# Kernel optimization log

Measured on AMD Instinct MI355X. Metric: run time of the kernel, lower is better.

The kernel has to match this reference:

```python
import jax, jax.numpy as jnp
import numpy as np

NUM_HEADS = 12
ROPE_THETA = 100.0

def _rotate_half(x):
    x1 = x[..., ::2]
    x2 = x[..., 1::2]
    return jnp.stack((-x2, x1), axis=-1).reshape(x.shape)

def _apply_rope(x, cos, sin):
    return x * cos + _rotate_half(x) * sin

def _rope_cos_sin(h, w, head_dim, theta):
    quarter = head_dim // 4  # head_dim=64 -> 16 freq bands
    inv_freq = 1.0 / theta ** (jnp.arange(quarter, dtype=jnp.float32) / max(quarter, 1))
    y = jnp.repeat(jnp.arange(h, dtype=jnp.float32), w)   # [h*w]
    xc = jnp.tile(jnp.arange(w, dtype=jnp.float32), h)    # [h*w]
    y_freqs = y[:, None] * inv_freq[None, :]               # [N, quarter]
    x_freqs = xc[:, None] * inv_freq[None, :]
    y_ang = jnp.repeat(y_freqs, 2, axis=-1)                # [N, half]
    x_ang = jnp.repeat(x_freqs, 2, axis=-1)
    ang = jnp.concatenate([y_ang, x_ang], axis=-1)         # [N, head_dim]
    return jnp.cos(ang)[None, None], jnp.sin(ang)[None, None]  # [1,1,N,hd]

def setup_inputs() -> dict:
    key = jax.random.key(0)
    ks = jax.random.split(key, 8)
    B, S, D = 8, 1025, 768
    s = 0.02
    return {
        "x": jax.random.normal(ks[0], (B, S, D), jnp.float32),
        "q_w": jax.random.normal(ks[1], (D, D), jnp.float32) * s,
        "q_b": jax.random.normal(ks[2], (D,), jnp.float32) * s,
        "k_w": jax.random.normal(ks[3], (D, D), jnp.float32) * s,
        "v_w": jax.random.normal(ks[4], (D, D), jnp.float32) * s,
        "v_b": jax.random.normal(ks[5], (D,), jnp.float32) * s,
        "o_w": jax.random.normal(ks[6], (D, D), jnp.float32) * s,
        "o_b": jax.random.normal(ks[7], (D,), jnp.float32) * s,
        "h": 32,
        "w": 32,
        "num_prefix_tokens": 1,
    }

def reference(x, q_w, q_b, k_w, v_w, v_b, o_w, o_b, h, w, num_prefix_tokens):
    B, S, D = x.shape
    H = NUM_HEADS
    hd = D // H
    scale = hd ** -0.5
    p = num_prefix_tokens

    def proj(W, b):
        y = jnp.einsum('bsd,ed->bse', x, W)
        if b is not None:
            y = y + b
        return y.reshape(B, S, H, hd).transpose(0, 2, 1, 3)  # [B,H,S,hd]

    q = proj(q_w, q_b)
    k = proj(k_w, None)
    v = proj(v_w, v_b)

    cos, sin = _rope_cos_sin(h, w, hd, ROPE_THETA)
    q = jnp.concatenate([q[:, :, :p], _apply_rope(q[:, :, p:], cos, sin)], axis=2)
    k = jnp.concatenate([k[:, :, :p], _apply_rope(k[:, :, p:], cos, sin)], axis=2)

    attn = jnp.einsum('bhqd,bhkd->bhqk', q * scale, k)
    attn = jax.nn.softmax(attn, axis=-1)
    out = jnp.einsum('bhqk,bhkd->bhqd', attn, v)
    out = out.transpose(0, 2, 1, 3).reshape(B, S, D)
    return jnp.einsum('bsd,ed->bse', out, o_w) + o_b
```

## Files before the change

### kernel.cpp

```cpp
#include <hip/hip_runtime.h>

typedef unsigned short u16;
typedef unsigned int   u32;
typedef __attribute__((ext_vector_type(4))) short s4;
typedef __attribute__((ext_vector_type(8))) short s8;
typedef __attribute__((ext_vector_type(4))) float f4;
typedef __attribute__((ext_vector_type(16))) float f16v;

#define NB   8
#define SEQ  1025
#define DIM  768
#define NH   12
#define HD   64
#define BPAD 1040
#define MPAD 8320
#define MV   8200
#define SQP  1040
#define SKP  1088
#define NG16 68
#define NQKV 2304
#define BHT  96
#define QSCALE 0.1803368801111204f

__device__ __forceinline__ u16 f2bf(float f) {
  u32 u = __builtin_bit_cast(u32, f);
  u += 0x7fffu + ((u >> 16) & 1u);
  return (u16)(u >> 16);
}
__device__ __forceinline__ float bf2f(u16 h) {
  return __builtin_bit_cast(float, ((u32)h) << 16);
}
__device__ __forceinline__ float exp2f_(float x) {
#if __has_builtin(__builtin_amdgcn_exp2f)
  return __builtin_amdgcn_exp2f(x);
#else
  return exp2f(x);
#endif
}
__device__ __forceinline__ u32 cvtpk(float a, float b) {
  u32 r;
  asm("v_cvt_pk_bf16_f32 %0, %1, %2" : "=v"(r) : "v"(a), "v"(b));
  return r;
}

typedef const __attribute__((address_space(1))) void cas1v;
typedef __attribute__((address_space(3))) void as3v;
__device__ __forceinline__ void gload16(const void* g, void* l) {
  __builtin_amdgcn_global_load_lds((cas1v*)g, (as3v*)l, 16, 0, 0);
}

#define MFMA16(a, b, c) __builtin_amdgcn_mfma_f32_16x16x32_bf16(a, b, c, 0, 0, 0)
#define MFMA32(a, b, c) __builtin_amdgcn_mfma_f32_32x32x16_bf16(a, b, c, 0, 0, 0)

__global__ void conv_all(const float* __restrict__ x,
                         const float* __restrict__ qw, const float* __restrict__ kw,
                         const float* __restrict__ vw, const float* __restrict__ ow,
                         const float* __restrict__ qb, const float* __restrict__ vb,
                         u16* __restrict__ xb,
                         u16* __restrict__ wqkv, u16* __restrict__ wo,
                         float* __restrict__ biasq, float2* __restrict__ rt) {
  if (blockIdx.x < 6240) {
    int i = blockIdx.x * 256 + threadIdx.x;
    int e = i * 4;
    int row = e / DIM, col = e - row * DIM;
    int b = row / BPAD, s = row - b * BPAD;
    s4 o;
    if (s < SEQ) {
      float4 v = *(const float4*)(x + ((size_t)(b * SEQ + s)) * DIM + col);
      o[0] = (short)f2bf(v.x); o[1] = (short)f2bf(v.y);
      o[2] = (short)f2bf(v.z); o[3] = (short)f2bf(v.w);
    } else {
      o = (s4){0, 0, 0, 0};
    }
    *(s4*)(xb + e) = o;
  } else {
    int i = (blockIdx.x - 6240) * 256 + threadIdx.x;
    wqkv[i]           = f2bf(qw[i]);
    wqkv[i + 589824]  = f2bf(kw[i]);
    wqkv[i + 1179648] = f2bf(vw[i]);
    wo[i]             = f2bf(ow[i]);
    if (i < NQKV) biasq[i] = (i < 768) ? qb[i] : (i < 1536 ? 0.f : vb[i - 1536]);
    if (i < SEQ * 32) {
      int s = i >> 5, jj = i & 31;
      float cs = 1.f, sn = 0.f;
      if (s > 0) {
        int tok = s - 1;
        int pos = (jj < 16) ? (tok >> 5) : (tok & 31);
        int f = jj & 15;
        float ang = (float)pos * __expf((float)f * -0.28782313662425572f);
        __sincosf(ang, &sn, &cs);
      }
      rt[i] = make_float2(cs, sn);
    }
  }
}

__global__ __launch_bounds__(512, 4) void gemm_qkv(const u16* __restrict__ A, const u16* __restrict__ Bm,
                                                   const float* __restrict__ bias,
                                                   u16* __restrict__ Ql, u16* __restrict__ Kl,
                                                   u16* __restrict__ Vp, const float2* __restrict__ rt) {
  __shared__ u16 smem[24576];
  const int K = DIM;
  int tid = threadIdx.x;
  int lane = tid & 63, wave = tid >> 6;
  int g = lane >> 4, c16 = lane & 15;
  int wm = wave >> 2, wn = wave & 3;
  int nwg = gridDim.x, orig = blockIdx.x;
  int qd = nwg >> 3, rm = nwg & 7, xcd = orig & 7;
  int wgid = (xcd < rm ? xcd * (qd + 1) : rm * (qd + 1) + (xcd - rm) * qd) + (orig >> 3);
  int m0 = (wgid / 9) * 128, n0 = (wgid % 9) * 256;
  f4 acc[4][4] = {};

  int ldrow = wave * 16 + (lane >> 2);
  int ldk = ((lane & 3) ^ ((ldrow >> 1) & 3)) * 8;
  const u16* Asrc = A + (size_t)(m0 + ldrow) * K + ldk;
  const u16* Bsrc = Bm + (size_t)(n0 + ldrow) * K + ldk;

  auto stage = [&](int buf, int k0) {
    gload16(Asrc + k0,           smem + buf * 4096 + wave * 512);
    gload16(Bsrc + k0,           smem + 8192 + buf * 8192 + wave * 512);
    gload16(Bsrc + 128 * K + k0, smem + 8192 + buf * 8192 + 4096 + wave * 512);
  };

  stage(0, 0);
  __syncthreads();
  int kx = (g ^ ((c16 >> 1) & 3)) * 8;
  for (int t = 0; t < 24; t++) {
    int buf = t & 1;
    if (t + 1 < 24) stage(buf ^ 1, (t + 1) << 5);
    s8 af[4], bf[4];
#pragma unroll
    for (int i = 0; i < 4; i++) {
      af[i] = *(const s8*)(smem + buf * 4096 + (wm * 64 + i * 16 + c16) * 32 + kx);
      bf[i] = *(const s8*)(smem + 8192 + buf * 8192 + (wn * 64 + i * 16 + c16) * 32 + kx);
    }
    __builtin_amdgcn_s_setprio(1);
#pragma unroll
    for (int i = 0; i < 4; i++)
#pragma unroll
      for (int j = 0; j < 4; j++)
        acc[i][j] = MFMA16(af[i], bf[j], acc[i][j]);
    __builtin_amdgcn_s_setprio(0);
    __syncthreads();
  }

  int part = (n0 >= 1536) ? 2 : (n0 >= 768 ? 1 : 0);
  float qs = (part == 0) ? QSCALE : 1.0f;
  u16 (*ct)[258] = (u16(*)[258])smem;
#pragma unroll
  for (int ih = 0; ih < 2; ih++) {
    __syncthreads();
#pragma unroll
    for (int j = 0; j < 4; j++) {
      int col = wn * 64 + j * 16 + c16;
      float bv = bias[n0 + col];
      int jj = (col & 63) >> 1;
      int odd = col & 1;
#pragma unroll
      for (int il = 0; il < 2; il++) {
        int i = ih * 2 + il;
        int lrow = wm * 32 + il * 16 + g * 4;
        int mrow = m0 + wm * 64 + i * 16 + g * 4;
#pragma unroll
        for (int r = 0; r < 4; r++) {
          float v = acc[i][j][r] + bv;
          u16 o;
          if (part < 2) {
            float vp = __shfl_xor(v, 1);
            int s = (mrow + r) % BPAD;
            float2 t = rt[(s < SEQ ? s : SEQ - 1) * 32 + jj];
            float rv = odd ? (v * t.x + vp * t.y) : (v * t.x - vp * t.y);
            o = f2bf(rv * qs);
          } else {
            o = f2bf(v);
          }
          ct[lrow + r][col] = o;
        }
      }
    }
    __syncthreads();
    if (part < 2) {
      u16* dstB = (part == 0) ? Ql : Kl;
      int stride = (part == 0) ? SQP : SKP;
#pragma unroll
      for (int p = 0; p < 4; p++) {
        int task = p * 512 + tid;
        int lrow = task >> 5, cg = (task & 31) * 8;
        int m = m0 + (lrow >> 5) * 64 + ih * 32 + (lrow & 31);
        int b = m / BPAD, s = m - b * BPAD;
        int n = n0 + cg;
        int hq = (n >> 6) - part * NH;
        s8 v = *(const s8*)&ct[lrow][cg];
        *(s8*)(dstB + ((size_t)((b * NH + hq) * stride + s)) * HD + (n & 63)) = v;
      }
    } else {
#pragma unroll
      for (int p = 0; p < 2; p++) {
        int task = p * 512 + tid;
        int col = task & 255, rg = task >> 8;
        int lbase = rg * 16;
        int mb = m0 + (lbase >> 5) * 64 + ih * 32 + (lbase & 31);
        int b = mb / BPAD, sb = mb - b * BPAD;
        int g16 = sb >> 4;
        int n = n0 + col;
        int hq = (n >> 6) - 2 * NH;
        s8 o0, o1;
#pragma unroll
        for (int k = 0; k < 16; k++) {
          int mp = (k & 3) | (((k >> 3) & 1) << 2) | (((k >> 2) & 1) << 3);
          u16 val = ct[lbase + k][col];
          if (mp < 8) o0[mp] = (short)val; else o1[mp - 8] = (short)val;
        }
        u16* dst = Vp + ((size_t)((b * NH + hq) * NG16 + g16) * HD + (n & 63)) * 16;
        *(s8*)dst = o0;
        *(s8*)(dst + 8) = o1;
      }
    }
  }
}

__global__ __launch_bounds__(256) void gemm_o(const u16* __restrict__ A, const u16* __restrict__ Bm,
                                              float* __restrict__ Cf, const float* __restrict__ bias,
                                              int N, int K, int Mvalid, int nnt) {
  __shared__ u16 smem[16384];
  int tid = threadIdx.x;
  int lane = tid & 63, wave = tid >> 6;
  int g = lane >> 4, c16 = lane & 15;
  int nwg = gridDim.x, orig = blockIdx.x;
  int qd = nwg >> 3, rm = nwg & 7, xcd = orig & 7;
  int wgid = (xcd < rm ? xcd * (qd + 1) : rm * (qd + 1) + (xcd - rm) * qd) + (orig >> 3);
  int m0 = (wgid / nnt) * 128, n0 = (wgid % nnt) * 128;
  int wm = wave >> 1, wn = wave & 1;
  f4 acc[4][4] = {};

  int ldrow = wave * 16 + (lane >> 2);
  int ldk = ((lane & 3) ^ ((ldrow >> 1) & 3)) * 8;
  const u16* Asrc = A + (size_t)(m0 + ldrow) * K + ldk;
  const u16* Bsrc = Bm + (size_t)(n0 + ldrow) * K + ldk;

  auto stage = [&](int buf, int k0) {
    u16* aw = smem + buf * 4096 + wave * 512;
    u16* bw = smem + 8192 + buf * 4096 + wave * 512;
    gload16(Asrc + k0, aw);
    gload16(Asrc + 64 * K + k0, aw + 2048);
    gload16(Bsrc + k0, bw);
    gload16(Bsrc + 64 * K + k0, bw + 2048);
  };

  stage(0, 0);
  __syncthreads();
  int nk = K >> 5;
  int kx = (g ^ ((c16 >> 1) & 3)) * 8;
  for (int t = 0; t < nk; t++) {
    int buf = t & 1;
    if (t + 1 < nk) stage(buf ^ 1, (t + 1) << 5);
    s8 af[4], bf[4];
#pragma unroll
    for (int i = 0; i < 4; i++) {
      af[i] = *(const s8*)(smem + buf * 4096 + (wm * 64 + i * 16 + c16) * 32 + kx);
      bf[i] = *(const s8*)(smem + 8192 + buf * 4096 + (wn * 64 + i * 16 + c16) * 32 + kx);
    }
    __builtin_amdgcn_s_setprio(1);
#pragma unroll
    for (int i = 0; i < 4; i++)
#pragma unroll
      for (int j = 0; j < 4; j++)
        acc[i][j] = MFMA16(af[i], bf[j], acc[i][j]);
    __builtin_amdgcn_s_setprio(0);
    __syncthreads();
  }

#pragma unroll
  for (int i = 0; i < 4; i++)
#pragma unroll
    for (int j = 0; j < 4; j++) {
      int n = n0 + wn * 64 + j * 16 + c16;
      float bv = bias[n];
#pragma unroll
      for (int r = 0; r < 4; r++) {
        int m = m0 + wm * 64 + i * 16 + g * 4 + r;
        if (m < Mvalid) Cf[(size_t)m * N + n] = acc[i][j][r] + bv;
      }
    }
}

__global__ __launch_bounds__(256) void attn_k(const u16* __restrict__ Q, const u16* __restrict__ K,
                                              const u16* __restrict__ Vp, u16* __restrict__ Ao) {
  __shared__ u16 lds[2][64 * 64];
  int bh = blockIdx.x;
  int tid = threadIdx.x;
  int wave = tid >> 6, lane = tid & 63;
  int q32 = lane & 31, h = lane >> 5;
  int b = bh / NH, hh = bh % NH;
  int qb = blockIdx.y * 128 + wave * 32;
  if (qb > SEQ - 32) qb = SEQ - 32;
  const u16* Qb = Q + (size_t)bh * SQP * HD;
  const u16* Kb = K + (size_t)bh * SKP * HD;
  const u16* Vb = Vp + (size_t)bh * NG16 * 1024 + 16 * q32 + 8 * h;

  s8 qf[4];
#pragma unroll
  for (int t = 0; t < 4; t++)
    qf[t] = *(const s8*)(Qb + (size_t)(qb + q32) * HD + 16 * t + 8 * h);

  f16v o0 = {}, o1 = {};
  float lrun = 0.f;
  int swz = (q32 & 7) << 4;

  auto stage = [&](int buf, int c) {
#pragma unroll
    for (int i = 0; i < 2; i++) {
      int sb = i * 4096 + tid * 16;
      int row = sb >> 7;
      int ch = (sb >> 4) & 7;
      int so = (ch ^ (row & 7)) * 8;
      u16* kd = &lds[buf][i * 2048 + wave * 512];
      gload16(Kb + (size_t)(c * 64 + row) * HD + so, kd);
    }
  };

  stage(0, 0);
  __syncthreads();

  for (int c = 0; c < 17; c++) {
    int buf = c & 1;
    s8 vf0[4], vf1[4];
    {
      const u16* vc = Vb + c * 4096;
#pragma unroll
      for (int s = 0; s < 4; s++) {
        vf0[s] = *(const s8*)(vc + 1024 * s);
        vf1[s] = *(const s8*)(vc + 1024 * s + 512);
      }
    }
    if (c < 16) stage(buf ^ 1, c + 1);
    const char* Ks = (const char*)&lds[buf][0];

    f16v st0 = {}, st1 = {};
    __builtin_amdgcn_s_setprio(1);
#pragma unroll
    for (int t = 0; t < 4; t++) {
      int off = (32 * t + 16 * h) ^ swz;
      s8 a0 = *(const s8*)(Ks + q32 * 128 + off);
      s8 a1 = *(const s8*)(Ks + (32 + q32) * 128 + off);
      st0 = MFMA32(a0, qf[t], st0);
      st1 = MFMA32(a1, qf[t], st1);
    }
    __builtin_amdgcn_s_setprio(0);

    if (c == 16) {
      st0[0] = h ? -3e38f : st0[0];
#pragma unroll
      for (int r = 1; r < 16; r++) st0[r] = -3e38f;
#pragma unroll
      for (int r = 0; r < 16; r++) st1[r] = -3e38f;
    }

    float sm[8];
#pragma unroll
    for (int r = 0; r < 16; r++) {
      st0[r] = exp2f_(st0[r]);
      st1[r] = exp2f_(st1[r]);
    }
#pragma unroll
    for (int r = 0; r < 8; r++) sm[r] = (st0[r] + st0[r + 8]) + (st1[r] + st1[r + 8]);
#pragma unroll
    for (int w = 4; w >= 1; w >>= 1)
#pragma unroll
      for (int r = 0; r < w; r++) sm[r] += sm[r + w];
    lrun += sm[0] + __shfl_xor(sm[0], 32);

    __builtin_amdgcn_s_setprio(1);
#pragma unroll
    for (int s = 0; s < 4; s++) {
      union { s8 v; u32 w[4]; } pa;
#pragma unroll
      for (int i = 0; i < 4; i++) {
        float plo = (s < 2) ? st0[8 * (s & 1) + 2 * i]     : st1[8 * (s & 1) + 2 * i];
        float phi = (s < 2) ? st0[8 * (s & 1) + 2 * i + 1] : st1[8 * (s & 1) + 2 * i + 1];
        pa.w[i] = cvtpk(plo, phi);
      }
      o0 = MFMA32(pa.v, vf0[s], o0);
      o1 = MFMA32(pa.v, vf1[s], o1);
    }
    __builtin_amdgcn_s_setprio(0);
    __syncthreads();
  }

  float rl = 1.0f / lrun;
#pragma unroll
  for (int r = 0; r < 16; r++) {
    int cr = (r & 3) + 8 * (r >> 2) + 4 * h;
    float sc = __shfl(rl, cr);
    u16* dst = Ao + (size_t)(b * SEQ + qb + cr) * DIM + hh * HD;
    dst[q32]      = f2bf(o0[r] * sc);
    dst[32 + q32] = f2bf(o1[r] * sc);
  }
}

extern "C" void kernel_launch(void* const* d_in, const int* in_sizes, int n_in,
                              void* d_out, int out_size, void* d_ws, size_t ws_size,
                              hipStream_t stream) {
  const float* x  = (const float*)d_in[0];
  const float* qw = (const float*)d_in[1];
  const float* qb = (const float*)d_in[2];
  const float* kw = (const float*)d_in[3];
  const float* vw = (const float*)d_in[4];
  const float* vb = (const float*)d_in[5];
  const float* ow = (const float*)d_in[6];
  const float* ob = (const float*)d_in[7];
  float* out = (float*)d_out;

  char* ws = (char*)d_ws;
  u16*    xb   = (u16*)(ws);
  u16*    wqkv = (u16*)(ws + 12779520);
  u16*    wo   = (u16*)(ws + 16318464);
  float*  bq   = (float*)(ws + 17498112);
  float2* rt   = (float2*)(ws + 17507328);
  u16*    Ql   = (u16*)(ws + 17769728);
  u16*    Kl   = (u16*)(ws + 30549248);
  u16*    Vp   = (u16*)(ws + 43918592);
  u16*    Ao   = xb;

  conv_all<<<8544, 256, 0, stream>>>(x, qw, kw, vw, ow, qb, vb, xb, wqkv, wo, bq, rt);
  gemm_qkv<<<585, 512, 0, stream>>>(xb, wqkv, bq, Ql, Kl, Vp, rt);
  attn_k<<<dim3(96, 9), 256, 0, stream>>>(Ql, Kl, Vp, Ao);
  gemm_o<<<390, 256, 0, stream>>>(Ao, wo, out, ob, DIM, DIM, MV, 6);
}
```

Measured before the change: 141.7 us.

## Double workgroup size for attention and output GEMM with larger tiles

The attention kernel moves to 512-thread blocks covering 256 queries each, so each staged K chunk is shared by twice as many waves and the grid shrinks to 96x5. The output projection GEMM moves to 512 threads with 128x256 tiles and hardcoded dimensions, so each A tile is reused across more columns. Both aim to cut redundant global and LDS traffic per output. In exchange there are fewer blocks (195 and 480), which risks lower occupancy, and the attention kernel now has more clamped, overlapping tail waves.

```diff
diff --git a/kernel.cpp b/kernel.cpp
--- a/kernel.cpp
+++ b/kernel.cpp
@@ -219,18 +219,18 @@
   }
 }
 
-__global__ __launch_bounds__(256) void gemm_o(const u16* __restrict__ A, const u16* __restrict__ Bm,
-                                              float* __restrict__ Cf, const float* __restrict__ bias,
-                                              int N, int K, int Mvalid, int nnt) {
-  __shared__ u16 smem[16384];
+__global__ __launch_bounds__(512, 4) void gemm_o(const u16* __restrict__ A, const u16* __restrict__ Bm,
+                                                 float* __restrict__ Cf, const float* __restrict__ bias) {
+  __shared__ u16 smem[24576];
+  const int K = DIM;
   int tid = threadIdx.x;
   int lane = tid & 63, wave = tid >> 6;
   int g = lane >> 4, c16 = lane & 15;
+  int wm = wave >> 2, wn = wave & 3;
   int nwg = gridDim.x, orig = blockIdx.x;
   int qd = nwg >> 3, rm = nwg & 7, xcd = orig & 7;
   int wgid = (xcd < rm ? xcd * (qd + 1) : rm * (qd + 1) + (xcd - rm) * qd) + (orig >> 3);
-  int m0 = (wgid / nnt) * 128, n0 = (wgid % nnt) * 128;
-  int wm = wave >> 1, wn = wave & 1;
+  int m0 = (wgid / 3) * 128, n0 = (wgid % 3) * 256;
   f4 acc[4][4] = {};
 
   int ldrow = wave * 16 + (lane >> 2);
@@ -239,26 +239,22 @@
   const u16* Bsrc = Bm + (size_t)(n0 + ldrow) * K + ldk;
 
   auto stage = [&](int buf, int k0) {
-    u16* aw = smem + buf * 4096 + wave * 512;
-    u16* bw = smem + 8192 + buf * 4096 + wave * 512;
-    gload16(Asrc + k0, aw);
-    gload16(Asrc + 64 * K + k0, aw + 2048);
-    gload16(Bsrc + k0, bw);
-    gload16(Bsrc + 64 * K + k0, bw + 2048);
+    gload16(Asrc + k0,           smem + buf * 4096 + wave * 512);
+    gload16(Bsrc + k0,           smem + 8192 + buf * 8192 + wave * 512);
+    gload16(Bsrc + 128 * K + k0, smem + 8192 + buf * 8192 + 4096 + wave * 512);
   };
 
   stage(0, 0);
   __syncthreads();
-  int nk = K >> 5;
   int kx = (g ^ ((c16 >> 1) & 3)) * 8;
-  for (int t = 0; t < nk; t++) {
+  for (int t = 0; t < 24; t++) {
     int buf = t & 1;
-    if (t + 1 < nk) stage(buf ^ 1, (t + 1) << 5);
+    if (t + 1 < 24) stage(buf ^ 1, (t + 1) << 5);
     s8 af[4], bf[4];
 #pragma unroll
     for (int i = 0; i < 4; i++) {
       af[i] = *(const s8*)(smem + buf * 4096 + (wm * 64 + i * 16 + c16) * 32 + kx);
-      bf[i] = *(const s8*)(smem + 8192 + buf * 4096 + (wn * 64 + i * 16 + c16) * 32 + kx);
+      bf[i] = *(const s8*)(smem + 8192 + buf * 8192 + (wn * 64 + i * 16 + c16) * 32 + kx);
     }
     __builtin_amdgcn_s_setprio(1);
 #pragma unroll
@@ -271,20 +267,21 @@
   }
 
 #pragma unroll
-  for (int i = 0; i < 4; i++)
-#pragma unroll
-    for (int j = 0; j < 4; j++) {
-      int n = n0 + wn * 64 + j * 16 + c16;
-      float bv = bias[n];
+  for (int j = 0; j < 4; j++) {
+    int n = n0 + wn * 64 + j * 16 + c16;
+    float bv = bias[n];
+#pragma unroll
+    for (int i = 0; i < 4; i++) {
 #pragma unroll
       for (int r = 0; r < 4; r++) {
         int m = m0 + wm * 64 + i * 16 + g * 4 + r;
-        if (m < Mvalid) Cf[(size_t)m * N + n] = acc[i][j][r] + bv;
-      }
-    }
-}
-
-__global__ __launch_bounds__(256) void attn_k(const u16* __restrict__ Q, const u16* __restrict__ K,
+        if (m < MV) Cf[(size_t)m * DIM + n] = acc[i][j][r] + bv;
+      }
+    }
+  }
+}
+
+__global__ __launch_bounds__(512) void attn_k(const u16* __restrict__ Q, const u16* __restrict__ K,
                                               const u16* __restrict__ Vp, u16* __restrict__ Ao) {
   __shared__ u16 lds[2][64 * 64];
   int bh = blockIdx.x;
@@ -292,7 +289,7 @@
   int wave = tid >> 6, lane = tid & 63;
   int q32 = lane & 31, h = lane >> 5;
   int b = bh / NH, hh = bh % NH;
-  int qb = blockIdx.y * 128 + wave * 32;
+  int qb = blockIdx.y * 256 + wave * 32;
   if (qb > SEQ - 32) qb = SEQ - 32;
   const u16* Qb = Q + (size_t)bh * SQP * HD;
   const u16* Kb = K + (size_t)bh * SKP * HD;
@@ -308,15 +305,11 @@
   int swz = (q32 & 7) << 4;
 
   auto stage = [&](int buf, int c) {
-#pragma unroll
-    for (int i = 0; i < 2; i++) {
-      int sb = i * 4096 + tid * 16;
-      int row = sb >> 7;
-      int ch = (sb >> 4) & 7;
-      int so = (ch ^ (row & 7)) * 8;
-      u16* kd = &lds[buf][i * 2048 + wave * 512];
-      gload16(Kb + (size_t)(c * 64 + row) * HD + so, kd);
-    }
+    int row = tid >> 3;
+    int ch = tid & 7;
+    int so = (ch ^ (row & 7)) * 8;
+    u16* kd = &lds[buf][tid * 8];
+    gload16(Kb + (size_t)(c * 64 + row) * HD + so, kd);
   };
 
   stage(0, 0);
@@ -424,6 +417,6 @@
 
   conv_all<<<8544, 256, 0, stream>>>(x, qw, kw, vw, ow, qb, vb, xb, wqkv, wo, bq, rt);
   gemm_qkv<<<585, 512, 0, stream>>>(xb, wqkv, bq, Ql, Kl, Vp, rt);
-  attn_k<<<dim3(96, 9), 256, 0, stream>>>(Ql, Kl, Vp, Ao);
-  gemm_o<<<390, 256, 0, stream>>>(Ao, wo, out, ob, DIM, DIM, MV, 6);
-}
+  attn_k<<<dim3(96, 5), 512, 0, stream>>>(Ql, Kl, Vp, Ao);
+  gemm_o<<<195, 512, 0, stream>>>(Ao, wo, out, ob);
+}
```

Measured after the change: 142.3 us. No clear change (+0.4%).
